# Kernel tuning notes

Measured on AMD Instinct MI355X. Metric: run time of the kernel, lower is better.

Reference implementation:

```python
import jax, jax.numpy as jnp
import numpy as np

H = 512      # hidden_size (hardcoded in prior split)
L = 3        # num_layers
NH = 8       # num_heads
B = 16384    # batch
LN_EPS = 1e-5


def layer_norm(x, g, b):
    m = x.mean(-1, keepdims=True)
    v = ((x - m) ** 2).mean(-1, keepdims=True)
    return (x - m) / jnp.sqrt(v + LN_EPS) * g + b


def cross_gen(src, tgt, ipw, ipb, qkv_w, qkv_b, ao_w, ao_b,
              ln1g, ln1b, ln2g, ln2b, f1w, f1b, f2w, f2b, opw, opb, rw):
    """CrossModalGenerator.forward(src, tgt) for the whole batch (seq_len == 1)."""
    bsz = src.shape[0]
    dh = H // NH
    x = src @ ipw.T + ipb  # input_proj
    for l in range(L):
        wq, wk, wv = jnp.split(qkv_w[l], 3, axis=0)
        bq, bk, bv = jnp.split(qkv_b[l], 3)
        q = (x @ wq.T + bq).reshape(bsz, NH, dh)
        k = (tgt @ wk.T + bk).reshape(bsz, NH, dh)
        v = (tgt @ wv.T + bv).reshape(bsz, NH, dh)
        # single key/value token -> softmax over 1 element == 1 (kept for faithful grads)
        scores = (q * k).sum(-1, keepdims=True) / jnp.sqrt(jnp.float32(dh))  # [B,NH,1]
        w = jax.nn.softmax(scores, axis=-1)
        attn = (w * v).reshape(bsz, H)
        attn = attn @ ao_w[l].T + ao_b[l]  # MHA out_proj
        x = layer_norm(x + attn, ln1g[l], ln1b[l])
        h = jax.nn.gelu(x @ f1w[l].T + f1b[l], approximate=False)
        h = h @ f2w[l].T + f2b[l]
        x = layer_norm(x + h, ln2g[l], ln2b[l])
    gen = x @ opw.T + opb  # output_proj
    return rw * tgt + (1.0 - rw) * gen


def setup_inputs() -> dict:
    key = jax.random.key(0)
    ks = iter(jax.random.split(key, 40))
    nk = lambda: next(ks)
    s = jnp.float32(0.02)  # weight scale for numerical sanity
    f32 = jnp.float32
    return {
        "image_features": jax.random.normal(nk(), (B, H), f32),
        "text_features": jax.random.normal(nk(), (B, H), f32),
        "g_ipw": jax.random.normal(nk(), (2, H, H), f32) * s,
        "g_ipb": jnp.zeros((2, H), f32),
        "g_qkv_w": jax.random.normal(nk(), (2, L, 3 * H, H), f32) * s,
        "g_qkv_b": jnp.zeros((2, L, 3 * H), f32),
        "g_ao_w": jax.random.normal(nk(), (2, L, H, H), f32) * s,
        "g_ao_b": jnp.zeros((2, L, H), f32),
        "g_ln1g": jnp.ones((2, L, H), f32),
        "g_ln1b": jnp.zeros((2, L, H), f32),
        "g_ln2g": jnp.ones((2, L, H), f32),
        "g_ln2b": jnp.zeros((2, L, H), f32),
        "g_f1w": jax.random.normal(nk(), (2, L, 4 * H, H), f32) * s,
        "g_f1b": jnp.zeros((2, L, 4 * H), f32),
        "g_f2w": jax.random.normal(nk(), (2, L, H, 4 * H), f32) * s,
        "g_f2b": jnp.zeros((2, L, H), f32),
        "g_opw": jax.random.normal(nk(), (2, H, H), f32) * s,
        "g_opb": jnp.zeros((2, H), f32),
        "g_rw": jnp.full((2,), 0.5, f32),  # residual_weight per generator
        "prior_w1": jax.random.normal(nk(), (2 * H, H), f32) * s,
        "prior_b1": jnp.zeros((2 * H,), f32),
        "prior_w2": jax.random.normal(nk(), (2 * H, 2 * H), f32) * s,
        "prior_b2": jnp.zeros((2 * H,), f32),
        "prior_emb": jax.random.normal(nk(), (1, H), f32),
        "missing_type": jax.random.randint(nk(), (B,), 0, 4, jnp.int32),
    }


def reference(image_features, text_features, g_ipw, g_ipb, g_qkv_w, g_qkv_b,
              g_ao_w, g_ao_b, g_ln1g, g_ln1b, g_ln2g, g_ln2b, g_f1w, g_f1b,
              g_f2w, g_f2b, g_opw, g_opb, g_rw, prior_w1, prior_b1, prior_w2,
              prior_b2, prior_emb, missing_type):
    def gen(i, src, tgt):
        return cross_gen(src, tgt, g_ipw[i], g_ipb[i], g_qkv_w[i], g_qkv_b[i],
                         g_ao_w[i], g_ao_b[i], g_ln1g[i], g_ln1b[i],
                         g_ln2g[i], g_ln2b[i], g_f1w[i], g_f1b[i],
                         g_f2w[i], g_f2b[i], g_opw[i], g_opb[i], g_rw[i])

    # MoE-style dense dispatch: run both generators on the full batch, select by type.
    gen_text = gen(0, image_features, text_features)  # img_to_text, missing_type==1
    gen_img = gen(1, text_features, image_features)   # text_to_img, missing_type==2

    prior = jax.nn.gelu(prior_emb @ prior_w1.T + prior_b1, approximate=False)
    prior = prior @ prior_w2.T + prior_b2  # [1, 2H]
    p_img, p_text = prior[:, :H], prior[:, H:]

    mt = missing_type[:, None]
    enhanced_img = jnp.where(mt == 2, gen_img, image_features)
    enhanced_img = jnp.where(mt == 3, p_img, enhanced_img)
    enhanced_text = jnp.where(mt == 1, gen_text, text_features)
    enhanced_text = jnp.where(mt == 3, p_text, enhanced_text)
    return enhanced_img, enhanced_text
```

## Files before the change

### kernel.cpp

```cpp
#include <hip/hip_runtime.h>
#include <hip/hip_bf16.h>
#include <math.h>

#define BDIM 16384
#define HDIM 512

typedef __bf16 bf16;
typedef float f32x4 __attribute__((ext_vector_type(4)));
typedef __bf16 bf16x8 __attribute__((ext_vector_type(8)));
typedef __bf16 bf16x4 __attribute__((ext_vector_type(4)));

#define WAITV(N) asm volatile("s_waitcnt vmcnt(" #N ")" ::: "memory")


__device__ __forceinline__ void gload16(const bf16* g, bf16* l) {
  __builtin_amdgcn_global_load_lds((const __attribute__((address_space(1))) void*)g,
                                   (__attribute__((address_space(3))) void*)l, 16, 0, 0);
}

__device__ __forceinline__ float gelu_exact(float x) {
  return 0.5f * x * (1.0f + erff(x * 0.70710678118654752f));
}
__device__ __forceinline__ float gelu_fast2(float x) {
  float x3 = x * x * x;
  float e = exp2f(fmaf(-0.1029432f, x3, -2.3022082f * x));
  return x * __builtin_amdgcn_rcpf(1.f + e);
}


__global__ void cvt_f32_bf16(const float* __restrict__ src, bf16* __restrict__ dst, int n4) {
  int i = blockIdx.x * blockDim.x + threadIdx.x;
  if (i >= n4) return;
  f32x4 v = *(const f32x4*)(src + (size_t)i * 4);
  bf16x4 o;
  o[0] = (bf16)v[0]; o[1] = (bf16)v[1]; o[2] = (bf16)v[2]; o[3] = (bf16)v[3];
  *(bf16x4*)(dst + (size_t)i * 4) = o;
}

__global__ void cvt_wvT(const float* __restrict__ qkv, bf16* __restrict__ dst) {
  __shared__ float t[32][33];
  int il = blockIdx.z;
  int bm = blockIdx.x * 32;
  int bk = blockIdx.y * 32;
  const float* s = qkv + (size_t)il * 786432 + 524288;
  int tx = threadIdx.x & 31, ty = threadIdx.x >> 5;
#pragma unroll
  for (int j = 0; j < 4; ++j)
    t[ty * 4 + j][tx] = s[(size_t)(bm + ty * 4 + j) * 512 + bk + tx];
  __syncthreads();
  bf16* d = dst + (size_t)il * 262144;
#pragma unroll
  for (int j = 0; j < 4; ++j)
    d[(size_t)(bk + ty * 4 + j) * 512 + bm + tx] = (bf16)t[tx][ty * 4 + j];
}

__global__ void zfill(float* __restrict__ p, int n) {
  int i = blockIdx.x * 256 + threadIdx.x;
  if (i < n) p[i] = 0.f;
}

__global__ void bias_combine(const float* __restrict__ aow, const float* __restrict__ qkvb,
                             const float* __restrict__ aob, float* __restrict__ bc) {
  int gid = blockIdx.x * 4 + (threadIdx.x >> 6);
  int il = gid >> 9;
  int lane = threadIdx.x & 63;
  const float* ar = aow + (size_t)gid * 512 + lane * 8;
  const float* bv = qkvb + il * 1536 + 1024 + lane * 8;
  float s = 0.f;
#pragma unroll
  for (int i = 0; i < 8; ++i) s += ar[i] * bv[i];
#pragma unroll
  for (int off = 32; off > 0; off >>= 1) s += __shfl_xor(s, off);
  if (lane == 0) bc[gid] = s + aob[gid];
}


template<int ACT, bool RES, int K>
__launch_bounds__(512, 1)
__global__ void gemm_8p(const bf16* __restrict__ A, long long Az,
                        const bf16* __restrict__ W, long long Wz,
                        const float* __restrict__ bias, long long bz,
                        const bf16* X, long long Xz,
                        bf16* C, long long Cz, int ldc) {
  __shared__ bf16 lds[65536];
  const long long z = blockIdx.z;
  A += z * Az; W += z * Wz; bias += z * bz; C += z * Cz;
  if (RES) X += z * Xz;
  const int tid = threadIdx.x, lane = tid & 63, wid = tid >> 6;
  const int brow = blockIdx.x * 256, bcol = blockIdx.y * 256;
  const int wm = (wid >> 2) * 128;
  const int wn = (wid & 3) * 64;
  const int lr = lane & 15, kg = lane >> 4;
  const int ko = (kg ^ ((lr >> 1) & 3)) << 3;

  f32x4 acc[8][4] = {};

  const int sco = (((tid & 3) ^ ((tid >> 3) & 3)) << 3);
  const bf16* Ag = A + (size_t)(brow + (tid >> 2)) * K + sco;
  const bf16* Wg = W + (size_t)(bcol + (tid >> 2)) * K + sco;
  const int nt = K / 64;

  auto STG = [&](const bf16* gbase, int kt, int kh, int dstE) {
    int ck = kt < nt ? kt : nt - 1;
    const bf16* s = gbase + (size_t)ck * 64 + (size_t)kh * 32;
    gload16(s, lds + dstE + wid * 512);
    gload16(s + (size_t)128 * K, lds + dstE + 4096 + wid * 512);
  };

  STG(Ag, 0, 0, 0);          STG(Wg, 0, 0, 16384);
  STG(Ag, 0, 1, 8192);       STG(Wg, 0, 1, 24576);
  STG(Ag, 1, 0, 32768);      STG(Wg, 1, 0, 32768 + 16384);

  bf16x8 a[8], b01[2], b23[2];

#define RD_A(BASE)                                                             \
  { _Pragma("unroll") for (int m = 0; m < 8; ++m)                              \
      a[m] = *(const bf16x8*)(lds + (BASE) + ((wm + m * 16 + lr) << 5) + ko); }
#define RD_B01(BASE)                                                           \
  { b01[0] = *(const bf16x8*)(lds + (BASE) + ((wn + lr) << 5) + ko);           \
    b01[1] = *(const bf16x8*)(lds + (BASE) + ((wn + 16 + lr) << 5) + ko); }
#define RD_B23(BASE)                                                           \
  { b23[0] = *(const bf16x8*)(lds + (BASE) + ((wn + 32 + lr) << 5) + ko);      \
    b23[1] = *(const bf16x8*)(lds + (BASE) + ((wn + 48 + lr) << 5) + ko); }
#define MM(N0, BB)                                                             \
  { __builtin_amdgcn_s_setprio(1);                                             \
    _Pragma("unroll") for (int m = 0; m < 8; ++m) {                            \
      acc[m][N0]     = __builtin_amdgcn_mfma_f32_16x16x32_bf16(BB[0], a[m], acc[m][N0], 0, 0, 0);     \
      acc[m][N0 + 1] = __builtin_amdgcn_mfma_f32_16x16x32_bf16(BB[1], a[m], acc[m][N0 + 1], 0, 0, 0); } \
    __builtin_amdgcn_s_setprio(0); }
#define BARW                                                                   \
  WAITV(6); __builtin_amdgcn_s_barrier(); asm volatile("" ::: "memory");
#define ENDP                                                                   \
  asm volatile("" ::: "memory"); __builtin_amdgcn_s_barrier();

  BARW
  RD_A(0) RD_B01(16384)

  const int niter = nt / 2;
  for (int i = 0; i < niter; ++i) {
    const int t = 2 * i;
    STG(Ag, t + 1, 1, 32768 + 8192);
    BARW  MM(0, b01)  RD_B23(16384)                      ENDP
    STG(Wg, t + 1, 1, 32768 + 24576);
    BARW  MM(2, b23)  RD_A(8192) RD_B01(24576)           ENDP
    STG(Ag, t + 2, 0, 0);
    BARW  MM(0, b01)  RD_B23(24576)                      ENDP
    STG(Wg, t + 2, 0, 16384);
    BARW  MM(2, b23)  RD_A(32768) RD_B01(49152)          ENDP
    STG(Ag, t + 2, 1, 8192);
    BARW  MM(0, b01)  RD_B23(49152)                      ENDP
    STG(Wg, t + 2, 1, 24576);
    BARW  MM(2, b23)  RD_A(40960) RD_B01(57344)          ENDP
    STG(Ag, t + 3, 0, 32768);
    BARW  MM(0, b01)  RD_B23(57344)                      ENDP
    STG(Wg, t + 3, 0, 32768 + 16384);
    BARW  MM(2, b23)  RD_A(0) RD_B01(16384)              ENDP
  }
#undef RD_A
#undef RD_B01
#undef RD_B23
#undef MM
#undef BARW
#undef ENDP

  f32x4 bv4[4];
#pragma unroll
  for (int n = 0; n < 4; ++n)
    bv4[n] = *(const f32x4*)(bias + bcol + wn + n * 16 + kg * 4);
#pragma unroll
  for (int m = 0; m < 8; ++m) {
    int row = brow + wm + m * 16 + lr;
#pragma unroll
    for (int n = 0; n < 4; ++n) {
      int col = bcol + wn + n * 16 + kg * 4;
      f32x4 v;
#pragma unroll
      for (int j = 0; j < 4; ++j) {
        float t2 = acc[m][n][j] + bv4[n][j];
        if (ACT == 1) t2 = gelu_fast2(t2);
        v[j] = t2;
      }
      if (RES) {
        bf16x4 xv = *(const bf16x4*)(X + (size_t)row * 512 + col);
#pragma unroll
        for (int j = 0; j < 4; ++j) v[j] += (float)xv[j];
      }
      bf16x4 o;
#pragma unroll
      for (int j = 0; j < 4; ++j) o[j] = (bf16)v[j];
      *(bf16x4*)(C + (size_t)row * ldc + col) = o;
    }
  }
}


template<int MODE>
__global__ void ln_chain(const bf16* __restrict__ Y, const bf16* __restrict__ R,
                         const float* __restrict__ gA, const float* __restrict__ bA,
                         const float* __restrict__ gB, const float* __restrict__ bB,
                         bf16* __restrict__ O) {
  int lane = threadIdx.x & 63;
  int row = blockIdx.x * 4 + (threadIdx.x >> 6);
  int gen = row >> 14;
  size_t base = (size_t)row * HDIM + lane * 8;
  bf16x8 yv = *(const bf16x8*)(Y + base);
  float v[8], s = 0.f, q = 0.f;
#pragma unroll
  for (int i = 0; i < 8; ++i) { v[i] = (float)yv[i]; s += v[i]; q += v[i] * v[i]; }
#pragma unroll
  for (int off = 32; off > 0; off >>= 1) { s += __shfl_xor(s, off); q += __shfl_xor(q, off); }
  float mean = s * (1.f / HDIM);
  float rstd = rsqrtf(q * (1.f / HDIM) - mean * mean + 1e-5f);
  const float* gAp = gA + gen * 1536 + lane * 8;
  const float* bAp = bA + gen * 1536 + lane * 8;
  if (MODE == 0) {
    bf16x8 o;
#pragma unroll
    for (int i = 0; i < 8; ++i) o[i] = (bf16)((v[i] - mean) * rstd * gAp[i] + bAp[i]);
    *(bf16x8*)(O + base) = o;
    return;
  }
  bf16x8 rv = *(const bf16x8*)(R + base);
  float u[8]; s = 0.f; q = 0.f;
#pragma unroll
  for (int i = 0; i < 8; ++i) {
    u[i] = (v[i] - mean) * rstd * gAp[i] + bAp[i] + (float)rv[i];
    s += u[i]; q += u[i] * u[i];
  }
#pragma unroll
  for (int off = 32; off > 0; off >>= 1) { s += __shfl_xor(s, off); q += __shfl_xor(q, off); }
  float m2 = s * (1.f / HDIM);
  float r2 = rsqrtf(q * (1.f / HDIM) - m2 * m2 + 1e-5f);
  const float* gBp = gB + gen * 1536 + lane * 8;
  const float* bBp = bB + gen * 1536 + lane * 8;
  bf16x8 o;
#pragma unroll
  for (int i = 0; i < 8; ++i) o[i] = (bf16)((u[i] - m2) * r2 * gBp[i] + bBp[i]);
  *(bf16x8*)(O + base) = o;
}


__launch_bounds__(256)
__global__ void gemm128(const bf16* __restrict__ A, long long Az, int lda,
                        const bf16* __restrict__ W, long long Wz,
                        const float* __restrict__ bias, long long bz,
                        bf16* __restrict__ C, long long Cz, int ldc, int K) {
  __shared__ bf16 As[128 * 64];
  __shared__ bf16 Bs[128 * 64];
  const long long z = blockIdx.z;
  A += z * Az; W += z * Wz; bias += z * bz; C += z * Cz;
  const int tid = threadIdx.x;
  const int lane = tid & 63;
  const int wid = tid >> 6;
  const int brow = blockIdx.x * 128;
  const int bcol = blockIdx.y * 128;
  const int wr = (wid >> 1) * 64;
  const int wc = (wid & 1) * 64;
  const int lr = lane & 15;
  const int kg = lane >> 4;
  f32x4 acc[4][4] = {};
  const bf16* Abase = A + (size_t)(brow + (tid >> 3)) * lda + ((tid & 7) << 3);
  const bf16* Wbase = W + (size_t)(bcol + (tid >> 3)) * K + ((tid & 7) << 3);
  bf16* AsDst = As + wid * 512;
  bf16* BsDst = Bs + wid * 512;
  for (int k0 = 0; k0 < K; k0 += 64) {
#pragma unroll
    for (int j = 0; j < 4; ++j) {
      gload16(Abase + (size_t)j * 32 * lda + k0, AsDst + j * 2048);
      gload16(Wbase + (size_t)j * 32 * K + k0, BsDst + j * 2048);
    }
    __syncthreads();
#pragma unroll
    for (int kk = 0; kk < 64; kk += 32) {
      bf16x8 a[4], bq[4];
#pragma unroll
      for (int m = 0; m < 4; ++m)
        a[m] = *(const bf16x8*)(As + (wr + m * 16 + lr) * 64 + kk + kg * 8);
#pragma unroll
      for (int n = 0; n < 4; ++n)
        bq[n] = *(const bf16x8*)(Bs + (wc + n * 16 + lr) * 64 + kk + kg * 8);
#pragma unroll
      for (int m = 0; m < 4; ++m)
#pragma unroll
        for (int n = 0; n < 4; ++n)
          acc[m][n] = __builtin_amdgcn_mfma_f32_16x16x32_bf16(a[m], bq[n], acc[m][n], 0, 0, 0);
    }
    __syncthreads();
  }
  float bv[4];
#pragma unroll
  for (int n = 0; n < 4; ++n) bv[n] = bias[bcol + wc + n * 16 + lr];
#pragma unroll
  for (int m = 0; m < 4; ++m) {
    int row = brow + wr + m * 16 + kg * 4;
#pragma unroll
    for (int n = 0; n < 4; ++n) {
      int col = bcol + wc + n * 16 + lr;
#pragma unroll
      for (int j = 0; j < 4; ++j)
        C[(size_t)(row + j) * ldc + col] = (bf16)(acc[m][n][j] + bv[n]);
    }
  }
}


__global__ void prior_fc1(const float* __restrict__ emb, const float* __restrict__ w1,
                          const float* __restrict__ b1, float* __restrict__ h) {
  int j = blockIdx.x * 4 + (threadIdx.x >> 6);
  int lane = threadIdx.x & 63;
  const float* wr = w1 + (size_t)j * 512 + lane * 8;
  const float* e = emb + lane * 8;
  float s = 0.f;
#pragma unroll
  for (int i = 0; i < 8; ++i) s += e[i] * wr[i];
#pragma unroll
  for (int off = 32; off > 0; off >>= 1) s += __shfl_xor(s, off);
  if (lane == 0) h[j] = gelu_exact(s + b1[j]);
}

__global__ void prior_fc2(const float* __restrict__ h, const float* __restrict__ w2,
                          const float* __restrict__ b2, float* __restrict__ p) {
  int j = blockIdx.x * 4 + (threadIdx.x >> 6);
  int lane = threadIdx.x & 63;
  const float* wr = w2 + (size_t)j * 1024 + lane * 16;
  const float* e = h + lane * 16;
  float s = 0.f;
#pragma unroll
  for (int i = 0; i < 16; ++i) s += e[i] * wr[i];
#pragma unroll
  for (int off = 32; off > 0; off >>= 1) s += __shfl_xor(s, off);
  if (lane == 0) p[j] = s + b2[j];
}


__global__ void combine(const float* __restrict__ img, const float* __restrict__ txt,
                        const bf16* __restrict__ gen_t, const bf16* __restrict__ gen_i,
                        const float* __restrict__ prior, const int* __restrict__ mt,
                        const float* __restrict__ rw, float* __restrict__ out) {
  int i4 = blockIdx.x * blockDim.x + threadIdx.x;
  if (i4 >= BDIM * 128) return;
  int bb = i4 >> 7;
  int c = (i4 & 127) << 2;
  size_t idx = (size_t)bb * HDIM + c;
  int m = mt[bb];
  f32x4 iv = *(const f32x4*)(img + idx);
  f32x4 tv = *(const f32x4*)(txt + idx);
  f32x4 oi = iv, ot = tv;
  if (m == 2) {
    float r = rw[1];
    bf16x4 gv = *(const bf16x4*)(gen_i + idx);
#pragma unroll
    for (int k = 0; k < 4; ++k) oi[k] = r * iv[k] + (1.f - r) * (float)gv[k];
  } else if (m == 3) {
    oi = *(const f32x4*)(prior + c);
  }
  if (m == 1) {
    float r = rw[0];
    bf16x4 gv = *(const bf16x4*)(gen_t + idx);
#pragma unroll
    for (int k = 0; k < 4; ++k) ot[k] = r * tv[k] + (1.f - r) * (float)gv[k];
  } else if (m == 3) {
    ot = *(const f32x4*)(prior + 512 + c);
  }
  *(f32x4*)(out + idx) = oi;
  *(f32x4*)(out + (size_t)BDIM * HDIM + idx) = ot;
}


extern "C" void kernel_launch(void* const* d_in, const int* in_sizes, int n_in,
                              void* d_out, int out_size, void* d_ws, size_t ws_size,
                              hipStream_t stream) {
  const float* img  = (const float*)d_in[0];
  const float* txt  = (const float*)d_in[1];
  const float* ipw  = (const float*)d_in[2];
  const float* ipb  = (const float*)d_in[3];
  const float* qkvw = (const float*)d_in[4];
  const float* qkvb = (const float*)d_in[5];
  const float* aow  = (const float*)d_in[6];
  const float* aob  = (const float*)d_in[7];
  const float* ln1g = (const float*)d_in[8];
  const float* ln1b = (const float*)d_in[9];
  const float* ln2g = (const float*)d_in[10];
  const float* ln2b = (const float*)d_in[11];
  const float* f1w  = (const float*)d_in[12];
  const float* f1b  = (const float*)d_in[13];
  const float* f2w  = (const float*)d_in[14];
  const float* f2b  = (const float*)d_in[15];
  const float* opw  = (const float*)d_in[16];
  const float* opb  = (const float*)d_in[17];
  const float* rw   = (const float*)d_in[18];
  const float* pw1  = (const float*)d_in[19];
  const float* pb1  = (const float*)d_in[20];
  const float* pw2  = (const float*)d_in[21];
  const float* pb2  = (const float*)d_in[22];
  const float* pemb = (const float*)d_in[23];
  const int*   mt   = (const int*)d_in[24];
  float* out = (float*)d_out;

  const size_t B = BDIM;
  char* ws = (char*)d_ws;
  size_t off = 0;
  auto alloc = [&](size_t bytes) -> char* {
    char* p = ws + off;
    off += (bytes + 255) & ~(size_t)255;
    return p;
  };
  bf16* src_bf = (bf16*)alloc(2 * B * 512 * 2);
  bf16* ipw_bf = (bf16*)alloc((size_t)2 * 262144 * 2);
  bf16* wvT_bf = (bf16*)alloc((size_t)6 * 262144 * 2);
  bf16* ao_bf  = (bf16*)alloc((size_t)6 * 262144 * 2);
  bf16* f1_bf  = (bf16*)alloc((size_t)6 * 1048576 * 2);
  bf16* f2_bf  = (bf16*)alloc((size_t)6 * 1048576 * 2);
  bf16* op_bf  = (bf16*)alloc((size_t)2 * 262144 * 2);
  bf16* Wc_bf  = (bf16*)alloc((size_t)6 * 262144 * 2);
  float* bc    = (float*)alloc(6 * 512 * 4);
  float* zeros = (float*)alloc(512 * 4);
  float* ph    = (float*)alloc(1024 * 4);
  float* pout  = (float*)alloc(1024 * 4);
  bf16* xn     = (bf16*)alloc(2 * B * 512 * 2);
  bf16* hreg   = (bf16*)alloc((size_t)B * 2048 * 2);
  bf16* h0     = (bf16*)d_out;
  const long long HZ = (long long)(hreg - h0);

  auto cvt = [&](const float* s, bf16* d, size_t n) {
    int n4 = (int)(n / 4);
    cvt_f32_bf16<<<(n4 + 255) / 256, 256, 0, stream>>>(s, d, n4);
  };
  cvt(img, src_bf, B * 512);
  cvt(txt, src_bf + B * 512, B * 512);
  cvt(ipw, ipw_bf, 2 * 262144);
  cvt(aow, ao_bf, 6 * 262144);
  cvt(f1w, f1_bf, 6 * 1048576);
  cvt(f2w, f2_bf, 6 * 1048576);
  cvt(opw, op_bf, 2 * 262144);
  cvt_wvT<<<dim3(16, 16, 6), 256, 0, stream>>>(qkvw, wvT_bf);
  zfill<<<2, 256, 0, stream>>>(zeros, 512);
  bias_combine<<<768, 256, 0, stream>>>(aow, qkvb, aob, bc);
  gemm128<<<dim3(4, 4, 6), 256, 0, stream>>>(ao_bf, 262144, 512, wvT_bf, 262144,
                                             zeros, 0, Wc_bf, 262144, 512, 512);
  prior_fc1<<<256, 256, 0, stream>>>(pemb, pw1, pb1, ph);
  prior_fc2<<<256, 256, 0, stream>>>(ph, pw2, pb2, pout);

  const long long BS = (long long)B * 512;

  auto attn = [&](int l) {
    gemm_8p<0, false, 512><<<dim3(64, 2, 2), 512, 0, stream>>>(
        src_bf + BS, -BS, Wc_bf + (size_t)l * 262144, 786432,
        bc + l * 512, 1536, nullptr, 0, hreg, BS, 512);
  };

  attn(0);
  gemm_8p<0, true, 512><<<dim3(64, 2, 2), 512, 0, stream>>>(
      src_bf, BS, ipw_bf, 262144, ipb, 512, hreg, BS, xn, BS, 512);
  ln_chain<0><<<2 * BDIM / 4, 256, 0, stream>>>(xn, nullptr, ln1g, ln1b,
                                                nullptr, nullptr, xn);

  for (int l = 0; l < 3; ++l) {
    gemm_8p<1, false, 512><<<dim3(64, 8, 2), 512, 0, stream>>>(
        xn, BS, f1_bf + (size_t)l * 1048576, 3145728,
        f1b + l * 2048, 6144, nullptr, 0, h0, HZ, 2048);
    gemm_8p<0, true, 2048><<<dim3(64, 2, 2), 512, 0, stream>>>(
        h0, HZ, f2_bf + (size_t)l * 1048576, 3145728,
        f2b + l * 512, 1536, xn, BS, xn, BS, 512);
    if (l < 2) {
      attn(l + 1);
      ln_chain<1><<<2 * BDIM / 4, 256, 0, stream>>>(
          xn, hreg, ln2g + l * 512, ln2b + l * 512,
          ln1g + (l + 1) * 512, ln1b + (l + 1) * 512, xn);
    } else {
      ln_chain<0><<<2 * BDIM / 4, 256, 0, stream>>>(
          xn, nullptr, ln2g + l * 512, ln2b + l * 512, nullptr, nullptr, xn);
    }
  }

  gemm_8p<0, false, 512><<<dim3(64, 2, 2), 512, 0, stream>>>(
      xn, BS, op_bf, 262144, opb, 512, nullptr, 0, hreg, BS, 512);

  combine<<<(BDIM * 128 + 255) / 256, 256, 0, stream>>>(img, txt, hreg, hreg + BS,
                                                        pout, mt, rw, out);
}
```

Baseline: 830.9 us.

## Fuse input projection with first attention GEMM and fold final combine into output GEMM

Concatenates image/text features into one [B,1024] bf16 buffer and builds concatenated weights and biases so the input projection and layer-0 attention become a single K=1024 GEMM per generator. This replaces two GEMMs plus a residual read. The output-projection GEMM now applies the residual-weight blend, missing-type selection and prior substitution in its epilogue and writes fp32 output directly, removing the separate combine kernel and the bf16 gen intermediate. It adds a few small prep kernels and a wider A stride. The fused epilogue writes fp32 from the GEMM, which may change its store pattern.

```diff
diff --git a/kernel.cpp b/kernel.cpp
--- a/kernel.cpp
+++ b/kernel.cpp
@@ -35,6 +35,43 @@
   bf16x4 o;
   o[0] = (bf16)v[0]; o[1] = (bf16)v[1]; o[2] = (bf16)v[2]; o[3] = (bf16)v[3];
   *(bf16x4*)(dst + (size_t)i * 4) = o;
+}
+
+__global__ void cvt_cat(const float* __restrict__ img, const float* __restrict__ txt,
+                        bf16* __restrict__ cat) {
+  int i = blockIdx.x * 256 + threadIdx.x;
+  int r = i >> 7;
+  int c = (i & 127) << 3;
+  const float* s = (c < 512) ? (img + (size_t)r * 512 + c)
+                             : (txt + (size_t)r * 512 + (c - 512));
+  f32x4 v0 = *(const f32x4*)s;
+  f32x4 v1 = *(const f32x4*)(s + 4);
+  bf16x8 o;
+#pragma unroll
+  for (int j = 0; j < 4; ++j) { o[j] = (bf16)v0[j]; o[4 + j] = (bf16)v1[j]; }
+  *(bf16x8*)(cat + (size_t)r * 1024 + c) = o;
+}
+
+__global__ void cat_w(const bf16* __restrict__ ipw_bf, const bf16* __restrict__ Wc_bf,
+                      bf16* __restrict__ Wcat) {
+  int i = blockIdx.x * 256 + threadIdx.x;
+  int g = i >> 16;
+  int rem = i & 65535;
+  int n = rem >> 7;
+  int c = (rem & 127) << 3;
+  const bf16* s;
+  if (g == 0) s = (c < 512) ? (ipw_bf + (size_t)n * 512 + c)
+                            : (Wc_bf + (size_t)n * 512 + (c - 512));
+  else        s = (c < 512) ? (Wc_bf + (size_t)3 * 262144 + (size_t)n * 512 + c)
+                            : (ipw_bf + 262144 + (size_t)n * 512 + (c - 512));
+  *(bf16x8*)(Wcat + (size_t)g * 524288 + (size_t)n * 1024 + c) = *(const bf16x8*)s;
+}
+
+__global__ void bcat_k(const float* __restrict__ ipb, const float* __restrict__ bc,
+                       float* __restrict__ bcat) {
+  int i = blockIdx.x * 256 + threadIdx.x;
+  int g = i >> 9, n = i & 511;
+  bcat[i] = ipb[g * 512 + n] + bc[g * 1536 + n];
 }
 
 __global__ void cvt_wvT(const float* __restrict__ qkv, bf16* __restrict__ dst) {
@@ -75,13 +112,16 @@
 }
 
 
-template<int ACT, bool RES, int K>
+template<int ACT, bool RES, int K, int FIN>
 __launch_bounds__(512, 1)
-__global__ void gemm_8p(const bf16* __restrict__ A, long long Az,
+__global__ void gemm_8p(const bf16* __restrict__ A, long long Az, int lda,
                         const bf16* __restrict__ W, long long Wz,
                         const float* __restrict__ bias, long long bz,
                         const bf16* X, long long Xz,
-                        bf16* C, long long Cz, int ldc) {
+                        bf16* C, long long Cz, int ldc,
+                        const float* imgF, const float* txtF,
+                        const float* prior, const int* mt,
+                        const float* rwp, float* outF) {
   __shared__ bf16 lds[65536];
   const long long z = blockIdx.z;
   A += z * Az; W += z * Wz; bias += z * bz; C += z * Cz;
@@ -96,20 +136,20 @@
   f32x4 acc[8][4] = {};
 
   const int sco = (((tid & 3) ^ ((tid >> 3) & 3)) << 3);
-  const bf16* Ag = A + (size_t)(brow + (tid >> 2)) * K + sco;
+  const bf16* Ag = A + (size_t)(brow + (tid >> 2)) * lda + sco;
   const bf16* Wg = W + (size_t)(bcol + (tid >> 2)) * K + sco;
   const int nt = K / 64;
 
-  auto STG = [&](const bf16* gbase, int kt, int kh, int dstE) {
+  auto STG = [&](const bf16* gbase, int kt, int kh, int dstE, int rstride) {
     int ck = kt < nt ? kt : nt - 1;
     const bf16* s = gbase + (size_t)ck * 64 + (size_t)kh * 32;
     gload16(s, lds + dstE + wid * 512);
-    gload16(s + (size_t)128 * K, lds + dstE + 4096 + wid * 512);
+    gload16(s + (size_t)128 * rstride, lds + dstE + 4096 + wid * 512);
   };
 
-  STG(Ag, 0, 0, 0);          STG(Wg, 0, 0, 16384);
-  STG(Ag, 0, 1, 8192);       STG(Wg, 0, 1, 24576);
-  STG(Ag, 1, 0, 32768);      STG(Wg, 1, 0, 32768 + 16384);
+  STG(Ag, 0, 0, 0, lda);         STG(Wg, 0, 0, 16384, K);
+  STG(Ag, 0, 1, 8192, lda);      STG(Wg, 0, 1, 24576, K);
+  STG(Ag, 1, 0, 32768, lda);     STG(Wg, 1, 0, 49152, K);
 
   bf16x8 a[8], b01[2], b23[2];
 
@@ -139,21 +179,21 @@
   const int niter = nt / 2;
   for (int i = 0; i < niter; ++i) {
     const int t = 2 * i;
-    STG(Ag, t + 1, 1, 32768 + 8192);
+    STG(Ag, t + 1, 1, 40960, lda);
     BARW  MM(0, b01)  RD_B23(16384)                      ENDP
-    STG(Wg, t + 1, 1, 32768 + 24576);
+    STG(Wg, t + 1, 1, 57344, K);
     BARW  MM(2, b23)  RD_A(8192) RD_B01(24576)           ENDP
-    STG(Ag, t + 2, 0, 0);
+    STG(Ag, t + 2, 0, 0, lda);
     BARW  MM(0, b01)  RD_B23(24576)                      ENDP
-    STG(Wg, t + 2, 0, 16384);
+    STG(Wg, t + 2, 0, 16384, K);
     BARW  MM(2, b23)  RD_A(32768) RD_B01(49152)          ENDP
-    STG(Ag, t + 2, 1, 8192);
+    STG(Ag, t + 2, 1, 8192, lda);
     BARW  MM(0, b01)  RD_B23(49152)                      ENDP
-    STG(Wg, t + 2, 1, 24576);
+    STG(Wg, t + 2, 1, 24576, K);
     BARW  MM(2, b23)  RD_A(40960) RD_B01(57344)          ENDP
-    STG(Ag, t + 3, 0, 32768);
+    STG(Ag, t + 3, 0, 32768, lda);
     BARW  MM(0, b01)  RD_B23(57344)                      ENDP
-    STG(Wg, t + 3, 0, 32768 + 16384);
+    STG(Wg, t + 3, 0, 49152, K);
     BARW  MM(2, b23)  RD_A(0) RD_B01(16384)              ENDP
   }
 #undef RD_A
@@ -167,6 +207,36 @@
 #pragma unroll
   for (int n = 0; n < 4; ++n)
     bv4[n] = *(const f32x4*)(bias + bcol + wn + n * 16 + kg * 4);
+
+  if constexpr (FIN == 1) {
+    float r = rwp[z];
+    const float* basep = z ? imgF : txtF;
+    const float* pr = prior + (z ? 0 : 512);
+    float* op2 = outF + (z ? (size_t)0 : (size_t)BDIM * HDIM);
+    const int want = z ? 2 : 1;
+#pragma unroll
+    for (int m = 0; m < 8; ++m) {
+      int row = brow + wm + m * 16 + lr;
+      int msel = mt[row];
+#pragma unroll
+      for (int n = 0; n < 4; ++n) {
+        int col = bcol + wn + n * 16 + kg * 4;
+        f32x4 base4 = *(const f32x4*)(basep + (size_t)row * 512 + col);
+        f32x4 o;
+#pragma unroll
+        for (int j = 0; j < 4; ++j) {
+          float g = acc[m][n][j] + bv4[n][j];
+          float ov = base4[j];
+          if (msel == want) ov = r * base4[j] + (1.f - r) * g;
+          else if (msel == 3) ov = pr[col + j];
+          o[j] = ov;
+        }
+        *(f32x4*)(op2 + (size_t)row * 512 + col) = o;
+      }
+    }
+    return;
+  }
+
 #pragma unroll
   for (int m = 0; m < 8; ++m) {
     int row = brow + wm + m * 16 + lr;
@@ -330,40 +400,6 @@
 #pragma unroll
   for (int off = 32; off > 0; off >>= 1) s += __shfl_xor(s, off);
   if (lane == 0) p[j] = s + b2[j];
-}
-
-
-__global__ void combine(const float* __restrict__ img, const float* __restrict__ txt,
-                        const bf16* __restrict__ gen_t, const bf16* __restrict__ gen_i,
-                        const float* __restrict__ prior, const int* __restrict__ mt,
-                        const float* __restrict__ rw, float* __restrict__ out) {
-  int i4 = blockIdx.x * blockDim.x + threadIdx.x;
-  if (i4 >= BDIM * 128) return;
-  int bb = i4 >> 7;
-  int c = (i4 & 127) << 2;
-  size_t idx = (size_t)bb * HDIM + c;
-  int m = mt[bb];
-  f32x4 iv = *(const f32x4*)(img + idx);
-  f32x4 tv = *(const f32x4*)(txt + idx);
-  f32x4 oi = iv, ot = tv;
-  if (m == 2) {
-    float r = rw[1];
-    bf16x4 gv = *(const bf16x4*)(gen_i + idx);
-#pragma unroll
-    for (int k = 0; k < 4; ++k) oi[k] = r * iv[k] + (1.f - r) * (float)gv[k];
-  } else if (m == 3) {
-    oi = *(const f32x4*)(prior + c);
-  }
-  if (m == 1) {
-    float r = rw[0];
-    bf16x4 gv = *(const bf16x4*)(gen_t + idx);
-#pragma unroll
-    for (int k = 0; k < 4; ++k) ot[k] = r * tv[k] + (1.f - r) * (float)gv[k];
-  } else if (m == 3) {
-    ot = *(const f32x4*)(prior + 512 + c);
-  }
-  *(f32x4*)(out + idx) = oi;
-  *(f32x4*)(out + (size_t)BDIM * HDIM + idx) = ot;
 }
 
 
@@ -405,7 +441,7 @@
     off += (bytes + 255) & ~(size_t)255;
     return p;
   };
-  bf16* src_bf = (bf16*)alloc(2 * B * 512 * 2);
+  bf16* cat    = (bf16*)alloc((size_t)B * 1024 * 2);
   bf16* ipw_bf = (bf16*)alloc((size_t)2 * 262144 * 2);
   bf16* wvT_bf = (bf16*)alloc((size_t)6 * 262144 * 2);
   bf16* ao_bf  = (bf16*)alloc((size_t)6 * 262144 * 2);
@@ -413,7 +449,9 @@
   bf16* f2_bf  = (bf16*)alloc((size_t)6 * 1048576 * 2);
   bf16* op_bf  = (bf16*)alloc((size_t)2 * 262144 * 2);
   bf16* Wc_bf  = (bf16*)alloc((size_t)6 * 262144 * 2);
+  bf16* Wcat   = (bf16*)alloc((size_t)2 * 524288 * 2);
   float* bc    = (float*)alloc(6 * 512 * 4);
+  float* bcat  = (float*)alloc(1024 * 4);
   float* zeros = (float*)alloc(512 * 4);
   float* ph    = (float*)alloc(1024 * 4);
   float* pout  = (float*)alloc(1024 * 4);
@@ -426,8 +464,7 @@
     int n4 = (int)(n / 4);
     cvt_f32_bf16<<<(n4 + 255) / 256, 256, 0, stream>>>(s, d, n4);
   };
-  cvt(img, src_bf, B * 512);
-  cvt(txt, src_bf + B * 512, B * 512);
+  cvt_cat<<<8192, 256, 0, stream>>>(img, txt, cat);
   cvt(ipw, ipw_bf, 2 * 262144);
   cvt(aow, ao_bf, 6 * 262144);
   cvt(f1w, f1_bf, 6 * 1048576);
@@ -438,30 +475,35 @@
   bias_combine<<<768, 256, 0, stream>>>(aow, qkvb, aob, bc);
   gemm128<<<dim3(4, 4, 6), 256, 0, stream>>>(ao_bf, 262144, 512, wvT_bf, 262144,
                                              zeros, 0, Wc_bf, 262144, 512, 512);
+  cat_w<<<512, 256, 0, stream>>>(ipw_bf, Wc_bf, Wcat);
+  bcat_k<<<4, 256, 0, stream>>>(ipb, bc, bcat);
   prior_fc1<<<256, 256, 0, stream>>>(pemb, pw1, pb1, ph);
   prior_fc2<<<256, 256, 0, stream>>>(ph, pw2, pb2, pout);
 
   const long long BS = (long long)B * 512;
 
   auto attn = [&](int l) {
-    gemm_8p<0, false, 512><<<dim3(64, 2, 2), 512, 0, stream>>>(
-        src_bf + BS, -BS, Wc_bf + (size_t)l * 262144, 786432,
-        bc + l * 512, 1536, nullptr, 0, hreg, BS, 512);
+    gemm_8p<0, false, 512, 0><<<dim3(64, 2, 2), 512, 0, stream>>>(
+        cat + 512, -512, 1024, Wc_bf + (size_t)l * 262144, 786432,
+        bc + l * 512, 1536, nullptr, 0, hreg, BS, 512,
+        nullptr, nullptr, nullptr, nullptr, nullptr, nullptr);
   };
 
-  attn(0);
-  gemm_8p<0, true, 512><<<dim3(64, 2, 2), 512, 0, stream>>>(
-      src_bf, BS, ipw_bf, 262144, ipb, 512, hreg, BS, xn, BS, 512);
+  gemm_8p<0, false, 1024, 0><<<dim3(64, 2, 2), 512, 0, stream>>>(
+      cat, 0, 1024, Wcat, 524288, bcat, 512, nullptr, 0, xn, BS, 512,
+      nullptr, nullptr, nullptr, nullptr, nullptr, nullptr);
   ln_chain<0><<<2 * BDIM / 4, 256, 0, stream>>>(xn, nullptr, ln1g, ln1b,
                                                 nullptr, nullptr, xn);
 
   for (int l = 0; l < 3; ++l) {
-    gemm_8p<1, false, 512><<<dim3(64, 8, 2), 512, 0, stream>>>(
-        xn, BS, f1_bf + (size_t)l * 1048576, 3145728,
-        f1b + l * 2048, 6144, nullptr, 0, h0, HZ, 2048);
-    gemm_8p<0, true, 2048><<<dim3(64, 2, 2), 512, 0, stream>>>(
-        h0, HZ, f2_bf + (size_t)l * 1048576, 3145728,
-        f2b + l * 512, 1536, xn, BS, xn, BS, 512);
+    gemm_8p<1, false, 512, 0><<<dim3(64, 8, 2), 512, 0, stream>>>(
+        xn, BS, 512, f1_bf + (size_t)l * 1048576, 3145728,
+        f1b + l * 2048, 6144, nullptr, 0, h0, HZ, 2048,
+        nullptr, nullptr, nullptr, nullptr, nullptr, nullptr);
+    gemm_8p<0, true, 2048, 0><<<dim3(64, 2, 2), 512, 0, stream>>>(
+        h0, HZ, 2048, f2_bf + (size_t)l * 1048576, 3145728,
+        f2b + l * 512, 1536, xn, BS, xn, BS, 512,
+        nullptr, nullptr, nullptr, nullptr, nullptr, nullptr);
     if (l < 2) {
       attn(l + 1);
       ln_chain<1><<<2 * BDIM / 4, 256, 0, stream>>>(
@@ -473,9 +515,7 @@
     }
   }
 
-  gemm_8p<0, false, 512><<<dim3(64, 2, 2), 512, 0, stream>>>(
-      xn, BS, op_bf, 262144, opb, 512, nullptr, 0, hreg, BS, 512);
-
-  combine<<<(BDIM * 128 + 255) / 256, 256, 0, stream>>>(img, txt, hreg, hreg + BS,
-                                                        pout, mt, rw, out);
-}
+  gemm_8p<0, false, 512, 1><<<dim3(64, 2, 2), 512, 0, stream>>>(
+      xn, BS, 512, op_bf, 262144, opb, 512, nullptr, 0, hreg, BS, 512,
+      img, txt, pout, mt, rw, out);
+}
```

New measurement: 819.1 us. Within noise of the previous version (-1.4%).
